# Kernel optimization log

Measured on AMD Instinct MI355X. Metric: run time of the kernel, lower is better.

## Reference

```python
import jax, jax.numpy as jnp
import numpy as np

N, F_IN, F_OUT, K = 16384, 64, 64, 3


def setup_inputs() -> dict:
    key = jax.random.key(0)
    k1, k2, k3, k4 = jax.random.split(key, 4)
    x = jax.random.normal(k1, (N, F_IN), dtype=jnp.float32)
    # dense rescaled Laplacian; scale so repeated matmuls stay numerically tame
    L_tilde = jax.random.normal(k2, (N, N), dtype=jnp.float32) / np.float32(np.sqrt(N))
    stdv = 1.0 / np.sqrt(F_OUT)
    weights = jax.random.uniform(k3, (K + 1, F_IN, F_OUT), dtype=jnp.float32,
                                 minval=-stdv, maxval=stdv)
    bias = jax.random.uniform(k4, (F_OUT,), dtype=jnp.float32, minval=-stdv, maxval=stdv)
    return {"x": x, "L_tilde": L_tilde, "weights": weights, "bias": bias}


def reference(x, L_tilde, weights, bias):
    # Chebyshev recurrence: T0 = x, T1 = L@x, Tk = 2*L@T_{k-1} - T_{k-2}
    T_prev = x                                   # (N, F_in)
    out = T_prev @ weights[0]                    # (N, F_out)
    T_curr = L_tilde @ x
    out = out + T_curr @ weights[1]
    for k in range(2, K + 1):                    # fixed small K: python loop is fine
        T_next = 2.0 * (L_tilde @ T_curr) - T_prev
        out = out + T_next @ weights[k]
        T_prev, T_curr = T_curr, T_next
    return out + bias
```

## Files before the change

### kernel.cpp

```cpp
#include <hip/hip_runtime.h>
#include <cstddef>
#include <cstdint>

#define NN 16384
#define FF 64
#define BM 64
#define BK 64
#define SK 4
#define KQ (NN / SK)
#define NC (KQ / BK)

typedef __attribute__((ext_vector_type(8))) short bf16x8;
typedef __attribute__((ext_vector_type(4))) float f32x4;
typedef unsigned short ushort_t;

#define GLOBAL_AS __attribute__((address_space(1)))
#define LDS_AS    __attribute__((address_space(3)))

__device__ __forceinline__ void f32_split(float f, ushort_t& h, ushort_t& l) {
    unsigned u = __builtin_bit_cast(unsigned, f);
    h = (ushort_t)(u >> 16);
    float hf = __builtin_bit_cast(float, u & 0xFFFF0000u);
    float lo = f - hf;
    l = (ushort_t)(__builtin_bit_cast(unsigned, lo) >> 16);
}

__global__ __launch_bounds__(256) void convT_init(
    const float* __restrict__ X, ushort_t* __restrict__ Th,
    ushort_t* __restrict__ Tl, const float* __restrict__ W0,
    const float* __restrict__ bias, float* __restrict__ out)
{
    __shared__ float S[64][68];
    __shared__ float W[64][64];
    const int t = threadIdx.x;
    const int rb = blockIdx.x * 64;
    {
        const int row = t >> 2;
        const int c0 = (t & 3) * 16;
        const float* src = X + (size_t)(rb + row) * FF + c0;
        *(float4*)&S[row][c0 + 0]  = *(const float4*)(src + 0);
        *(float4*)&S[row][c0 + 4]  = *(const float4*)(src + 4);
        *(float4*)&S[row][c0 + 8]  = *(const float4*)(src + 8);
        *(float4*)&S[row][c0 + 12] = *(const float4*)(src + 12);
        float4* wd = (float4*)&W[0][0];
        const float4* ws = (const float4*)W0;
#pragma unroll
        for (int j = 0; j < 4; ++j) wd[t * 4 + j] = ws[t * 4 + j];
    }
    __syncthreads();
    {
        const int cc = t >> 2;
        const int r0 = (t & 3) * 16;
        ushort_t hh[16], ll[16];
#pragma unroll
        for (int i = 0; i < 16; ++i) f32_split(S[r0 + i][cc], hh[i], ll[i]);
        unsigned wh[8], wl[8];
#pragma unroll
        for (int j = 0; j < 8; ++j) {
            wh[j] = (unsigned)hh[2 * j] | ((unsigned)hh[2 * j + 1] << 16);
            wl[j] = (unsigned)ll[2 * j] | ((unsigned)ll[2 * j + 1] << 16);
        }
        const size_t o = (size_t)cc * NN + rb + r0;
        *(uint4*)(Th + o)     = make_uint4(wh[0], wh[1], wh[2], wh[3]);
        *(uint4*)(Th + o + 8) = make_uint4(wh[4], wh[5], wh[6], wh[7]);
        *(uint4*)(Tl + o)     = make_uint4(wl[0], wl[1], wl[2], wl[3]);
        *(uint4*)(Tl + o + 8) = make_uint4(wl[4], wl[5], wl[6], wl[7]);
    }
    {
        const int row0 = (t >> 3) * 2;
        const int col0 = (t & 7) * 8;
        float acc[2][8];
        const float4 b0 = *(const float4*)(bias + col0);
        const float4 b1 = *(const float4*)(bias + col0 + 4);
#pragma unroll
        for (int r = 0; r < 2; ++r) {
            acc[r][0] = b0.x; acc[r][1] = b0.y; acc[r][2] = b0.z; acc[r][3] = b0.w;
            acc[r][4] = b1.x; acc[r][5] = b1.y; acc[r][6] = b1.z; acc[r][7] = b1.w;
        }
#pragma unroll
        for (int f = 0; f < FF; ++f) {
            const float x0 = S[row0][f];
            const float x1 = S[row0 + 1][f];
            const float4 w0 = *(const float4*)&W[f][col0];
            const float4 w1 = *(const float4*)&W[f][col0 + 4];
            acc[0][0] += x0 * w0.x; acc[0][1] += x0 * w0.y;
            acc[0][2] += x0 * w0.z; acc[0][3] += x0 * w0.w;
            acc[0][4] += x0 * w1.x; acc[0][5] += x0 * w1.y;
            acc[0][6] += x0 * w1.z; acc[0][7] += x0 * w1.w;
            acc[1][0] += x1 * w0.x; acc[1][1] += x1 * w0.y;
            acc[1][2] += x1 * w0.z; acc[1][3] += x1 * w0.w;
            acc[1][4] += x1 * w1.x; acc[1][5] += x1 * w1.y;
            acc[1][6] += x1 * w1.z; acc[1][7] += x1 * w1.w;
        }
#pragma unroll
        for (int r = 0; r < 2; ++r) {
            const size_t o = (size_t)(rb + row0 + r) * FF + col0;
            float4 v0, v1;
            v0.x = acc[r][0]; v0.y = acc[r][1]; v0.z = acc[r][2]; v0.w = acc[r][3];
            v1.x = acc[r][4]; v1.y = acc[r][5]; v1.z = acc[r][6]; v1.w = acc[r][7];
            *(float4*)(out + o) = v0;
            *(float4*)(out + o + 4) = v1;
        }
    }
}

__global__ __launch_bounds__(256) void cheb_gemm_mfma(
    const float* __restrict__ L, const ushort_t* __restrict__ Th,
    const ushort_t* __restrict__ Tl, float* __restrict__ P)
{
    __shared__ ushort_t Ah[2][BM * BK];
    __shared__ ushort_t Al[2][BM * BK];
    __shared__ ushort_t Bh[2][FF * BK];
    __shared__ ushort_t Bl[2][FF * BK];

    const int tid  = threadIdx.x;
    const int lane = tid & 63;
    const int w    = tid >> 6;
    const int s    = blockIdx.x >> 8;
    const int m    = blockIdx.x & 255;
    const int row0g = m * BM;
    const int kbase = s * KQ;

    const int wm = w >> 1, wn = w & 1;
    const int frow = lane & 15;
    const int fk8  = (lane >> 4) * 8;

    const int arow = w * 4 + (lane >> 4);
    const int akq  = lane & 15;
    const int axor = (arow & 7) << 4;

    const ushort_t* Tsrc = (w & 1) ? Tl : Th;
    const int boct0 = (w >> 1) * 4;

    f32x4 acc[2][2];
#pragma unroll
    for (int i = 0; i < 2; ++i)
#pragma unroll
        for (int j = 0; j < 2; ++j) acc[i][j] = (f32x4)0.f;

    float4 vaA[8], vaB[8];

    const float* Labase = L + (size_t)(row0g + arow) * NN + kbase + akq * 4;

#define ISSUE_B(c, slot)                                                        \
    {                                                                           \
        const size_t kc = (size_t)(c) * BK;                                     \
        char* bbase = (char*)((w & 1) ? Bl[slot] : Bh[slot]);                   \
        _Pragma("unroll")                                                       \
        for (int o = 0; o < 4; ++o) {                                           \
            const int oct = boct0 + o;                                          \
            const int col = oct * 8 + (lane >> 3);                              \
            const ushort_t* g = Tsrc + (size_t)col * NN + kbase + kc            \
                                + (((lane & 7) ^ (col & 7)) * 8);               \
            __builtin_amdgcn_global_load_lds((const GLOBAL_AS void*)g,          \
                (LDS_AS void*)(bbase + oct * 1024), 16, 0, 0);                  \
        }                                                                       \
    }

#define LOAD_PAIR(va, c)                                                        \
    {                                                                           \
        const float* g = Labase + (size_t)(c) * BK;                             \
        va[0] = *(const float4*)(g);                                            \
        va[1] = *(const float4*)(g + BK);                                       \
        va[2] = *(const float4*)(g + (size_t)16 * NN);                          \
        va[3] = *(const float4*)(g + (size_t)16 * NN + BK);                     \
        va[4] = *(const float4*)(g + (size_t)32 * NN);                          \
        va[5] = *(const float4*)(g + (size_t)32 * NN + BK);                     \
        va[6] = *(const float4*)(g + (size_t)48 * NN);                          \
        va[7] = *(const float4*)(g + (size_t)48 * NN + BK);                     \
    }

#define CONV_WRITE_A(va, j, slot)                                               \
    {                                                                           \
        char* ahb = (char*)Ah[slot];                                            \
        char* alb = (char*)Al[slot];                                            \
        _Pragma("unroll")                                                       \
        for (int p = 0; p < 4; ++p) {                                           \
            const float4 v = va[p * 2 + (j)];                                   \
            const int r = arow + p * 16;                                        \
            ushort_t h0, h1, h2, h3, l0, l1, l2, l3;                            \
            f32_split(v.x, h0, l0);                                             \
            f32_split(v.y, h1, l1);                                             \
            f32_split(v.z, h2, l2);                                             \
            f32_split(v.w, h3, l3);                                             \
            const unsigned hi01 = (unsigned)h0 | ((unsigned)h1 << 16);          \
            const unsigned hi23 = (unsigned)h2 | ((unsigned)h3 << 16);          \
            const unsigned lo01 = (unsigned)l0 | ((unsigned)l1 << 16);          \
            const unsigned lo23 = (unsigned)l2 | ((unsigned)l3 << 16);          \
            const int byte = (r * 128 + akq * 8) ^ axor;                        \
            *(uint2*)(ahb + byte) = make_uint2(hi01, hi23);                     \
            *(uint2*)(alb + byte) = make_uint2(lo01, lo23);                     \
        }                                                                       \
    }

#define COMPUTE(slot)                                                           \
    {                                                                           \
        const char* ahb = (const char*)Ah[slot];                                \
        const char* alb = (const char*)Al[slot];                                \
        const char* bhb = (const char*)Bh[slot];                                \
        const char* blb = (const char*)Bl[slot];                                \
        _Pragma("unroll")                                                       \
        for (int ks = 0; ks < 2; ++ks) {                                        \
            const int kk = ks * 32 + fk8;                                       \
            bf16x8 Afh[2], Afl[2], Bfh[2], Bfl[2];                              \
            _Pragma("unroll")                                                   \
            for (int mt = 0; mt < 2; ++mt) {                                    \
                const int row = wm * 32 + mt * 16 + frow;                       \
                const int off = (row * 128 + kk * 2) ^ ((row & 7) << 4);        \
                Afh[mt] = *(const bf16x8*)(ahb + off);                          \
                Afl[mt] = *(const bf16x8*)(alb + off);                          \
            }                                                                   \
            _Pragma("unroll")                                                   \
            for (int nt = 0; nt < 2; ++nt) {                                    \
                const int col = wn * 32 + nt * 16 + frow;                       \
                const int off = (col * 128 + kk * 2) ^ ((col & 7) << 4);        \
                Bfh[nt] = *(const bf16x8*)(bhb + off);                          \
                Bfl[nt] = *(const bf16x8*)(blb + off);                          \
            }                                                                   \
            _Pragma("unroll")                                                   \
            for (int mt = 0; mt < 2; ++mt)                                      \
                _Pragma("unroll")                                               \
                for (int nt = 0; nt < 2; ++nt) {                                \
                    acc[mt][nt] = __builtin_amdgcn_mfma_f32_16x16x32_bf16(      \
                        Afh[mt], Bfh[nt], acc[mt][nt], 0, 0, 0);                \
                    acc[mt][nt] = __builtin_amdgcn_mfma_f32_16x16x32_bf16(      \
                        Afh[mt], Bfl[nt], acc[mt][nt], 0, 0, 0);                \
                    acc[mt][nt] = __builtin_amdgcn_mfma_f32_16x16x32_bf16(      \
                        Afl[mt], Bfh[nt], acc[mt][nt], 0, 0, 0);                \
                }                                                               \
        }                                                                       \
    }

    ISSUE_B(0, 0)
    LOAD_PAIR(vaA, 0)
    CONV_WRITE_A(vaA, 0, 0)
    __syncthreads();

#pragma unroll 1
    for (int c = 0; c < NC; c += 4) {
        ISSUE_B(c + 1, 1)
        if (c + 2 < NC) LOAD_PAIR(vaB, c + 2)
        COMPUTE(0)
        CONV_WRITE_A(vaA, 1, 1)
        __syncthreads();
        if (c + 2 < NC) ISSUE_B(c + 2, 0)
        COMPUTE(1)
        if (c + 2 < NC) CONV_WRITE_A(vaB, 0, 0)
        __syncthreads();
        if (c + 2 >= NC) break;
        ISSUE_B(c + 3, 1)
        if (c + 4 < NC) LOAD_PAIR(vaA, c + 4)
        COMPUTE(0)
        CONV_WRITE_A(vaB, 1, 1)
        __syncthreads();
        if (c + 4 < NC) ISSUE_B(c + 4, 0)
        COMPUTE(1)
        if (c + 4 < NC) CONV_WRITE_A(vaA, 0, 0)
        __syncthreads();
    }

    float* Pp = P + (size_t)s * NN * FF;
#pragma unroll
    for (int mt = 0; mt < 2; ++mt)
#pragma unroll
        for (int nt = 0; nt < 2; ++nt) {
            const int row = row0g + wm * 32 + mt * 16 + (lane >> 4) * 4;
            const int col = wn * 32 + nt * 16 + frow;
#pragma unroll
            for (int r = 0; r < 4; ++r)
                Pp[(size_t)(row + r) * FF + col] = acc[mt][nt][r];
        }
#undef ISSUE_B
#undef LOAD_PAIR
#undef CONV_WRITE_A
#undef COMPUTE
}

__global__ __launch_bounds__(256) void post_hop(
    const float* __restrict__ P,
    const float* __restrict__ Tsub, const float* __restrict__ Wk,
    float* __restrict__ Tstore, ushort_t* __restrict__ Thn,
    ushort_t* __restrict__ Tln, float* __restrict__ out,
    float alpha, float beta)
{
    __shared__ float ST[64][33];
    __shared__ float WK[64][64];
    const int t = threadIdx.x;
    const int rb = blockIdx.x * 32;
    const size_t M1 = (size_t)NN * FF;

    {
        float4* wd = (float4*)&WK[0][0];
        const float4* ws = (const float4*)Wk;
#pragma unroll
        for (int j = 0; j < 4; ++j) wd[t * 4 + j] = ws[t * 4 + j];
    }

    const int row = t >> 3;
    const int c0 = (t & 7) * 8;
    const size_t o = (size_t)(rb + row) * FF + c0;

    {
        float tv[8];
#pragma unroll
        for (int half = 0; half < 2; ++half) {
            const size_t oo = o + 4 * half;
            float4 a0 = *(const float4*)(P + oo);
            const float4 a1 = *(const float4*)(P + M1 + oo);
            const float4 a2 = *(const float4*)(P + 2 * M1 + oo);
            const float4 a3 = *(const float4*)(P + 3 * M1 + oo);
            a0.x += a1.x + a2.x + a3.x; a0.y += a1.y + a2.y + a3.y;
            a0.z += a1.z + a2.z + a3.z; a0.w += a1.w + a2.w + a3.w;
            tv[4 * half + 0] = alpha * a0.x; tv[4 * half + 1] = alpha * a0.y;
            tv[4 * half + 2] = alpha * a0.z; tv[4 * half + 3] = alpha * a0.w;
        }
        if (beta != 0.f) {
            const float4 s0 = *(const float4*)(Tsub + o);
            const float4 s1 = *(const float4*)(Tsub + o + 4);
            tv[0] += beta * s0.x; tv[1] += beta * s0.y;
            tv[2] += beta * s0.z; tv[3] += beta * s0.w;
            tv[4] += beta * s1.x; tv[5] += beta * s1.y;
            tv[6] += beta * s1.z; tv[7] += beta * s1.w;
        }
        if (Tstore) {
            float4 v0, v1;
            v0.x = tv[0]; v0.y = tv[1]; v0.z = tv[2]; v0.w = tv[3];
            v1.x = tv[4]; v1.y = tv[5]; v1.z = tv[6]; v1.w = tv[7];
            *(float4*)(Tstore + o) = v0;
            *(float4*)(Tstore + o + 4) = v1;
        }
#pragma unroll
        for (int j = 0; j < 8; ++j) ST[c0 + j][row] = tv[j];
    }
    __syncthreads();

    if (Thn) {
        const int f = t >> 2;
        const int r0 = (t & 3) * 8;
        ushort_t hh[8], ll[8];
#pragma unroll
        for (int i = 0; i < 8; ++i) f32_split(ST[f][r0 + i], hh[i], ll[i]);
        unsigned wh[4], wl[4];
#pragma unroll
        for (int j = 0; j < 4; ++j) {
            wh[j] = (unsigned)hh[2 * j] | ((unsigned)hh[2 * j + 1] << 16);
            wl[j] = (unsigned)ll[2 * j] | ((unsigned)ll[2 * j + 1] << 16);
        }
        const size_t ob = (size_t)f * NN + rb + r0;
        *(uint4*)(Thn + ob) = make_uint4(wh[0], wh[1], wh[2], wh[3]);
        *(uint4*)(Tln + ob) = make_uint4(wl[0], wl[1], wl[2], wl[3]);
    }

    {
        float4 a0 = *(const float4*)(out + o);
        float4 a1 = *(const float4*)(out + o + 4);
#pragma unroll
        for (int f = 0; f < FF; ++f) {
            const float sv = ST[f][row];
            const float4 w0 = *(const float4*)&WK[f][c0];
            const float4 w1 = *(const float4*)&WK[f][c0 + 4];
            a0.x += sv * w0.x; a0.y += sv * w0.y;
            a0.z += sv * w0.z; a0.w += sv * w0.w;
            a1.x += sv * w1.x; a1.y += sv * w1.y;
            a1.z += sv * w1.z; a1.w += sv * w1.w;
        }
        *(float4*)(out + o) = a0;
        *(float4*)(out + o + 4) = a1;
    }
}

extern "C" void kernel_launch(void* const* d_in, const int* in_sizes, int n_in,
                              void* d_out, int out_size, void* d_ws, size_t ws_size,
                              hipStream_t stream)
{
    const float* x    = (const float*)d_in[0];
    const float* L    = (const float*)d_in[1];
    const float* W    = (const float*)d_in[2];
    const float* bias = (const float*)d_in[3];
    float* out = (float*)d_out;

    const size_t M1 = (size_t)NN * FF;
    float* wsf = (float*)d_ws;
    float* T1 = wsf;
    float* P  = wsf + M1;
    ushort_t* ThA = (ushort_t*)(wsf + 5 * M1);
    ushort_t* TlA = ThA + M1;
    ushort_t* ThB = TlA + M1;
    ushort_t* TlB = ThB + M1;

    const dim3 gc(NN / 64), bc(256);
    const dim3 gg(SK * 256), bg(256);
    const dim3 gp(NN / 32), bp(256);

    convT_init<<<gc, bc, 0, stream>>>(x, ThA, TlA, W + 0 * FF * FF, bias, out);
    cheb_gemm_mfma<<<gg, bg, 0, stream>>>(L, ThA, TlA, P);
    post_hop<<<gp, bp, 0, stream>>>(P, x, W + 1 * FF * FF,
                                    T1, ThB, TlB, out, 1.f, 0.f);
    cheb_gemm_mfma<<<gg, bg, 0, stream>>>(L, ThB, TlB, P);
    post_hop<<<gp, bp, 0, stream>>>(P, x, W + 2 * FF * FF,
                                    nullptr, ThA, TlA, out, 2.f, -1.f);
    cheb_gemm_mfma<<<gg, bg, 0, stream>>>(L, ThA, TlA, P);
    post_hop<<<gp, bp, 0, stream>>>(P, T1, W + 3 * FF * FF,
                                    nullptr, nullptr, nullptr, out, 2.f, -1.f);
}
```

Before: 693.8 us.

## Fuse split-K reduction and post-hop epilogue into GEMM via last-block atomic counter

Removes the separate post_hop kernel. Each split-K GEMM block increments a per-row-tile counter, and the last of the four blocks to finish does the reduction, Chebyshev combine, bf16 hi/lo split, and output projection. Counters are zeroed in convT_init. It also adds a launch-bounds occupancy hint of 2 and an XOR-swizzled LDS transpose buffer. This saves three kernel launches and their tail gaps, at the cost of a serialized epilogue on the last-arriving blocks and a possible register-pressure change from the occupancy hint.

```diff
diff --git a/kernel.cpp b/kernel.cpp
--- a/kernel.cpp
+++ b/kernel.cpp
@@ -17,6 +17,8 @@
 #define GLOBAL_AS __attribute__((address_space(1)))
 #define LDS_AS    __attribute__((address_space(3)))
 
+#define STIDX(f, r) ((f) * 64 + ((r) ^ (((f) & 15) << 2)))
+
 __device__ __forceinline__ void f32_split(float f, ushort_t& h, ushort_t& l) {
     unsigned u = __builtin_bit_cast(unsigned, f);
     h = (ushort_t)(u >> 16);
@@ -28,12 +30,14 @@
 __global__ __launch_bounds__(256) void convT_init(
     const float* __restrict__ X, ushort_t* __restrict__ Th,
     ushort_t* __restrict__ Tl, const float* __restrict__ W0,
-    const float* __restrict__ bias, float* __restrict__ out)
+    const float* __restrict__ bias, float* __restrict__ out,
+    int* __restrict__ cnt)
 {
     __shared__ float S[64][68];
     __shared__ float W[64][64];
     const int t = threadIdx.x;
     const int rb = blockIdx.x * 64;
+    if (t < 3) cnt[t * 256 + blockIdx.x] = 0;
     {
         const int row = t >> 2;
         const int c0 = (t & 3) * 16;
@@ -104,14 +108,20 @@
     }
 }
 
-__global__ __launch_bounds__(256) void cheb_gemm_mfma(
+__global__ __launch_bounds__(256, 2) void cheb_gemm_mfma(
     const float* __restrict__ L, const ushort_t* __restrict__ Th,
-    const ushort_t* __restrict__ Tl, float* __restrict__ P)
+    const ushort_t* __restrict__ Tl, float* __restrict__ P,
+    int* __restrict__ cnt,
+    const float* __restrict__ Tsub, const float* __restrict__ Wk,
+    float* __restrict__ Tstore, ushort_t* __restrict__ Thn,
+    ushort_t* __restrict__ Tln, float* __restrict__ out,
+    float alpha, float beta)
 {
     __shared__ ushort_t Ah[2][BM * BK];
     __shared__ ushort_t Al[2][BM * BK];
     __shared__ ushort_t Bh[2][FF * BK];
     __shared__ ushort_t Bl[2][FF * BK];
+    __shared__ int lastFlag;
 
     const int tid  = threadIdx.x;
     const int lane = tid & 63;
@@ -120,6 +130,7 @@
     const int m    = blockIdx.x & 255;
     const int row0g = m * BM;
     const int kbase = s * KQ;
+    const size_t M1 = (size_t)NN * FF;
 
     const int wm = w >> 1, wn = w & 1;
     const int frow = lane & 15;
@@ -259,114 +270,112 @@
         __syncthreads();
     }
 
-    float* Pp = P + (size_t)s * NN * FF;
-#pragma unroll
-    for (int mt = 0; mt < 2; ++mt)
-#pragma unroll
-        for (int nt = 0; nt < 2; ++nt) {
-            const int row = row0g + wm * 32 + mt * 16 + (lane >> 4) * 4;
-            const int col = wn * 32 + nt * 16 + frow;
-#pragma unroll
-            for (int r = 0; r < 4; ++r)
-                Pp[(size_t)(row + r) * FF + col] = acc[mt][nt][r];
-        }
+    {
+        float* Pp = P + (size_t)s * M1;
+#pragma unroll
+        for (int mt = 0; mt < 2; ++mt)
+#pragma unroll
+            for (int nt = 0; nt < 2; ++nt) {
+                const int row = row0g + wm * 32 + mt * 16 + (lane >> 4) * 4;
+                const int col = wn * 32 + nt * 16 + frow;
+#pragma unroll
+                for (int r = 0; r < 4; ++r)
+                    Pp[(size_t)(row + r) * FF + col] = acc[mt][nt][r];
+            }
+    }
+
+    __syncthreads();
+    if (tid == 0) {
+        __threadfence();
+        const int old = atomicAdd(cnt + m, 1);
+        const int last = (old == SK - 1) ? 1 : 0;
+        if (last) __threadfence();
+        lastFlag = last;
+    }
+    __syncthreads();
+    if (!lastFlag) return;
+
+    float* ST  = (float*)&Ah[0][0];
+    float* WKs = (float*)&Bh[0][0];
+
+    {
+        float4* wd = (float4*)WKs;
+        const float4* ws = (const float4*)Wk;
+#pragma unroll
+        for (int j = 0; j < 4; ++j) wd[tid * 4 + j] = ws[tid * 4 + j];
+    }
+
+    const int trow = tid >> 2;
+    const int tc0  = (tid & 3) * 16;
+    const size_t obase = (size_t)(row0g + trow) * FF + tc0;
+
+#pragma unroll
+    for (int j = 0; j < 4; ++j) {
+        const size_t oo = obase + 4 * j;
+        float4 a0 = *(const float4*)(P + oo);
+        const float4 a1 = *(const float4*)(P + M1 + oo);
+        const float4 a2 = *(const float4*)(P + 2 * M1 + oo);
+        const float4 a3 = *(const float4*)(P + 3 * M1 + oo);
+        a0.x += a1.x + a2.x + a3.x; a0.y += a1.y + a2.y + a3.y;
+        a0.z += a1.z + a2.z + a3.z; a0.w += a1.w + a2.w + a3.w;
+        float4 tv;
+        tv.x = alpha * a0.x; tv.y = alpha * a0.y;
+        tv.z = alpha * a0.z; tv.w = alpha * a0.w;
+        if (beta != 0.f) {
+            const float4 s0 = *(const float4*)(Tsub + oo);
+            tv.x += beta * s0.x; tv.y += beta * s0.y;
+            tv.z += beta * s0.z; tv.w += beta * s0.w;
+        }
+        if (Tstore) *(float4*)(Tstore + oo) = tv;
+        const int f0 = tc0 + 4 * j;
+        ST[STIDX(f0 + 0, trow)] = tv.x;
+        ST[STIDX(f0 + 1, trow)] = tv.y;
+        ST[STIDX(f0 + 2, trow)] = tv.z;
+        ST[STIDX(f0 + 3, trow)] = tv.w;
+    }
+    __syncthreads();
+
+    if (Thn) {
+        const int f = tid >> 2;
+        const int r0 = (tid & 3) * 16;
+        ushort_t hh[16], ll[16];
+#pragma unroll
+        for (int i = 0; i < 16; ++i)
+            f32_split(ST[STIDX(f, r0 + i)], hh[i], ll[i]);
+        unsigned wh[8], wl[8];
+#pragma unroll
+        for (int j = 0; j < 8; ++j) {
+            wh[j] = (unsigned)hh[2 * j] | ((unsigned)hh[2 * j + 1] << 16);
+            wl[j] = (unsigned)ll[2 * j] | ((unsigned)ll[2 * j + 1] << 16);
+        }
+        const size_t ob = (size_t)f * NN + row0g + r0;
+        *(uint4*)(Thn + ob)     = make_uint4(wh[0], wh[1], wh[2], wh[3]);
+        *(uint4*)(Thn + ob + 8) = make_uint4(wh[4], wh[5], wh[6], wh[7]);
+        *(uint4*)(Tln + ob)     = make_uint4(wl[0], wl[1], wl[2], wl[3]);
+        *(uint4*)(Tln + ob + 8) = make_uint4(wl[4], wl[5], wl[6], wl[7]);
+    }
+
+    {
+        float4 a[4];
+#pragma unroll
+        for (int j = 0; j < 4; ++j) a[j] = *(const float4*)(out + obase + 4 * j);
+#pragma unroll
+        for (int f = 0; f < FF; ++f) {
+            const float sv = ST[STIDX(f, trow)];
+#pragma unroll
+            for (int j = 0; j < 4; ++j) {
+                const float4 wv = *(const float4*)&WKs[f * 64 + tc0 + 4 * j];
+                a[j].x += sv * wv.x; a[j].y += sv * wv.y;
+                a[j].z += sv * wv.z; a[j].w += sv * wv.w;
+            }
+        }
+#pragma unroll
+        for (int j = 0; j < 4; ++j) *(float4*)(out + obase + 4 * j) = a[j];
+    }
 #undef ISSUE_B
 #undef LOAD_PAIR
 #undef CONV_WRITE_A
 #undef COMPUTE
-}
-
-__global__ __launch_bounds__(256) void post_hop(
-    const float* __restrict__ P,
-    const float* __restrict__ Tsub, const float* __restrict__ Wk,
-    float* __restrict__ Tstore, ushort_t* __restrict__ Thn,
-    ushort_t* __restrict__ Tln, float* __restrict__ out,
-    float alpha, float beta)
-{
-    __shared__ float ST[64][33];
-    __shared__ float WK[64][64];
-    const int t = threadIdx.x;
-    const int rb = blockIdx.x * 32;
-    const size_t M1 = (size_t)NN * FF;
-
-    {
-        float4* wd = (float4*)&WK[0][0];
-        const float4* ws = (const float4*)Wk;
-#pragma unroll
-        for (int j = 0; j < 4; ++j) wd[t * 4 + j] = ws[t * 4 + j];
-    }
-
-    const int row = t >> 3;
-    const int c0 = (t & 7) * 8;
-    const size_t o = (size_t)(rb + row) * FF + c0;
-
-    {
-        float tv[8];
-#pragma unroll
-        for (int half = 0; half < 2; ++half) {
-            const size_t oo = o + 4 * half;
-            float4 a0 = *(const float4*)(P + oo);
-            const float4 a1 = *(const float4*)(P + M1 + oo);
-            const float4 a2 = *(const float4*)(P + 2 * M1 + oo);
-            const float4 a3 = *(const float4*)(P + 3 * M1 + oo);
-            a0.x += a1.x + a2.x + a3.x; a0.y += a1.y + a2.y + a3.y;
-            a0.z += a1.z + a2.z + a3.z; a0.w += a1.w + a2.w + a3.w;
-            tv[4 * half + 0] = alpha * a0.x; tv[4 * half + 1] = alpha * a0.y;
-            tv[4 * half + 2] = alpha * a0.z; tv[4 * half + 3] = alpha * a0.w;
-        }
-        if (beta != 0.f) {
-            const float4 s0 = *(const float4*)(Tsub + o);
-            const float4 s1 = *(const float4*)(Tsub + o + 4);
-            tv[0] += beta * s0.x; tv[1] += beta * s0.y;
-            tv[2] += beta * s0.z; tv[3] += beta * s0.w;
-            tv[4] += beta * s1.x; tv[5] += beta * s1.y;
-            tv[6] += beta * s1.z; tv[7] += beta * s1.w;
-        }
-        if (Tstore) {
-            float4 v0, v1;
-            v0.x = tv[0]; v0.y = tv[1]; v0.z = tv[2]; v0.w = tv[3];
-            v1.x = tv[4]; v1.y = tv[5]; v1.z = tv[6]; v1.w = tv[7];
-            *(float4*)(Tstore + o) = v0;
-            *(float4*)(Tstore + o + 4) = v1;
-        }
-#pragma unroll
-        for (int j = 0; j < 8; ++j) ST[c0 + j][row] = tv[j];
-    }
-    __syncthreads();
-
-    if (Thn) {
-        const int f = t >> 2;
-        const int r0 = (t & 3) * 8;
-        ushort_t hh[8], ll[8];
-#pragma unroll
-        for (int i = 0; i < 8; ++i) f32_split(ST[f][r0 + i], hh[i], ll[i]);
-        unsigned wh[4], wl[4];
-#pragma unroll
-        for (int j = 0; j < 4; ++j) {
-            wh[j] = (unsigned)hh[2 * j] | ((unsigned)hh[2 * j + 1] << 16);
-            wl[j] = (unsigned)ll[2 * j] | ((unsigned)ll[2 * j + 1] << 16);
-        }
-        const size_t ob = (size_t)f * NN + rb + r0;
-        *(uint4*)(Thn + ob) = make_uint4(wh[0], wh[1], wh[2], wh[3]);
-        *(uint4*)(Tln + ob) = make_uint4(wl[0], wl[1], wl[2], wl[3]);
-    }
-
-    {
-        float4 a0 = *(const float4*)(out + o);
-        float4 a1 = *(const float4*)(out + o + 4);
-#pragma unroll
-        for (int f = 0; f < FF; ++f) {
-            const float sv = ST[f][row];
-            const float4 w0 = *(const float4*)&WK[f][c0];
-            const float4 w1 = *(const float4*)&WK[f][c0 + 4];
-            a0.x += sv * w0.x; a0.y += sv * w0.y;
-            a0.z += sv * w0.z; a0.w += sv * w0.w;
-            a1.x += sv * w1.x; a1.y += sv * w1.y;
-            a1.z += sv * w1.z; a1.w += sv * w1.w;
-        }
-        *(float4*)(out + o) = a0;
-        *(float4*)(out + o + 4) = a1;
-    }
 }
 
 extern "C" void kernel_launch(void* const* d_in, const int* in_sizes, int n_in,
@@ -387,19 +396,19 @@
     ushort_t* TlA = ThA + M1;
     ushort_t* ThB = TlA + M1;
     ushort_t* TlB = ThB + M1;
+    int* cnt = (int*)(wsf + 9 * M1);
 
     const dim3 gc(NN / 64), bc(256);
     const dim3 gg(SK * 256), bg(256);
-    const dim3 gp(NN / 32), bp(256);
-
-    convT_init<<<gc, bc, 0, stream>>>(x, ThA, TlA, W + 0 * FF * FF, bias, out);
-    cheb_gemm_mfma<<<gg, bg, 0, stream>>>(L, ThA, TlA, P);
-    post_hop<<<gp, bp, 0, stream>>>(P, x, W + 1 * FF * FF,
-                                    T1, ThB, TlB, out, 1.f, 0.f);
-    cheb_gemm_mfma<<<gg, bg, 0, stream>>>(L, ThB, TlB, P);
-    post_hop<<<gp, bp, 0, stream>>>(P, x, W + 2 * FF * FF,
-                                    nullptr, ThA, TlA, out, 2.f, -1.f);
-    cheb_gemm_mfma<<<gg, bg, 0, stream>>>(L, ThA, TlA, P);
-    post_hop<<<gp, bp, 0, stream>>>(P, T1, W + 3 * FF * FF,
-                                    nullptr, nullptr, nullptr, out, 2.f, -1.f);
+
+    convT_init<<<gc, bc, 0, stream>>>(x, ThA, TlA, W + 0 * FF * FF, bias, out, cnt);
+    cheb_gemm_mfma<<<gg, bg, 0, stream>>>(L, ThA, TlA, P, cnt + 0,
+                                          x, W + 1 * FF * FF,
+                                          T1, ThB, TlB, out, 1.f, 0.f);
+    cheb_gemm_mfma<<<gg, bg, 0, stream>>>(L, ThB, TlB, P, cnt + 256,
+                                          x, W + 2 * FF * FF,
+                                          nullptr, ThA, TlA, out, 2.f, -1.f);
+    cheb_gemm_mfma<<<gg, bg, 0, stream>>>(L, ThA, TlA, P, cnt + 512,
+                                          T1, W + 3 * FF * FF,
+                                          nullptr, nullptr, nullptr, out, 2.f, -1.f);
 }
```

New measurement: 862.2 us. 1.24x slower.
